# Kernel optimization log

Measured on AMD Instinct MI355X. Metric: run time of the kernel, lower is better.

## Reference

```python
import jax, jax.numpy as jnp
import numpy as np

B0, C0, H0, W0 = 2, 64, 48, 48
BR, DI, NS, RK, K = 128, 128, 16, 4, 4
EPS = 1e-5


def _bn_relu(x, g, b):
    # eval-mode BatchNorm2d (running mean 0, var 1) followed by ReLU; x is NCHW
    return jax.nn.relu(x * (g / jnp.sqrt(1.0 + EPS))[None, :, None, None] + b[None, :, None, None])


def _c1(x, w):
    # 1x1 conv, w: (O, C, 1, 1)
    return jnp.einsum('bchw,oc->bohw', x, w[:, :, 0, 0])


def _avgpool(x, k, s, p):
    # torch AvgPool2d with count_include_pad=True -> divide by k*k
    y = jax.lax.reduce_window(x, 0.0, jax.lax.add, (1, 1, k, k), (1, 1, s, s), ((0, 0), (0, 0), (p, p), (p, p)))
    return y / float(k * k)


def _resize(x, h, w):
    # bilinear, align_corners=False (half-pixel), NCHW
    return jax.image.resize(x, (x.shape[0], x.shape[1], h, w), 'bilinear')


def _pappm(x, s0_g, s0_b, s0_w, s1_g, s1_b, s1_w, s2_g, s2_b, s2_w, s3_g, s3_b, s3_w, s4_g, s4_b, s4_w, comp_g, comp_b, comp_w, sc_g, sc_b, sc_w):
    h, w = x.shape[2], x.shape[3]
    x0 = _c1(_bn_relu(x, s0_g, s0_b), s0_w)
    y1 = _c1(_bn_relu(_avgpool(x, 3, 1, 1), s1_g, s1_b), s1_w) + x0  # stride-1 pool keeps size
    y2 = _resize(_c1(_bn_relu(_avgpool(x, 5, 2, 2), s2_g, s2_b), s2_w), h, w) + x0
    y3 = _resize(_c1(_bn_relu(_avgpool(x, 9, 4, 4), s3_g, s3_b), s3_w), h, w) + x0
    y4 = _c1(_bn_relu(x.mean((2, 3), keepdims=True), s4_g, s4_b), s4_w) + x0  # 1x1 -> broadcast
    cat = jnp.concatenate([x0, y1, y2, y3, y4], axis=1)  # (B, 5*BR, H, W)
    comp = jax.lax.conv_general_dilated(_bn_relu(cat, comp_g, comp_b), comp_w, (1, 1), ((1, 1), (1, 1)), dimension_numbers=('NCHW', 'OIHW', 'NCHW'))
    return comp + _c1(_bn_relu(x, sc_g, sc_b), sc_w)


def _ss2d(xin, in_proj_w, dw_w, dw_b, x_proj_w, dt_w, dt_b, A_logs, Ds, ln_g, ln_b, out_proj_w):
    # xin: (B, H, W, d_model)
    Bb, Hh, Ww, _ = xin.shape
    xz = xin @ in_proj_w.T                      # (B,H,W,2*DI)
    xc, z = jnp.split(xz, 2, axis=-1)
    xc = jnp.transpose(xc, (0, 3, 1, 2))        # (B,DI,H,W)
    xc = jax.lax.conv_general_dilated(xc, dw_w, (1, 1), ((1, 1), (1, 1)), dimension_numbers=('NCHW', 'OIHW', 'NCHW'), feature_group_count=DI)
    xc = jax.nn.silu(xc + dw_b[None, :, None, None])
    L = Hh * Ww
    x_hw = xc.reshape(Bb, DI, L)
    x_wh = jnp.transpose(xc, (0, 1, 3, 2)).reshape(Bb, DI, L)
    xs = jnp.stack([x_hw, x_wh, x_hw[:, :, ::-1], x_wh[:, :, ::-1]], axis=1)  # (B,K,DI,L)
    x_dbl = jnp.einsum('bkdl,kcd->bkcl', xs, x_proj_w)
    dts, Bm, Cm = jnp.split(x_dbl, [RK, RK + NS], axis=2)  # (B,K,RK,L),(B,K,NS,L),(B,K,NS,L)
    delta = jax.nn.softplus(jnp.einsum('bkrl,kdr->bkdl', dts, dt_w) + dt_b[None, :, :, None])  # (B,K,DI,L)
    A = -jnp.exp(A_logs).reshape(K, DI, NS)
    a = jnp.exp(delta[..., None] * A[None, :, :, None, :])                    # (B,K,DI,L,NS)
    bu = (delta * xs)[..., None] * jnp.transpose(Bm, (0, 1, 3, 2))[:, :, None]  # (B,K,DI,L,NS)

    def comb(e1, e2):
        a1, b1 = e1
        a2, b2 = e2
        return a2 * a1, a2 * b1 + b2

    _, hst = jax.lax.associative_scan(comb, (a, bu), axis=3)  # h_t = a_t*h_{t-1} + b_t
    y = jnp.einsum('bkdln,bknl->bkdl', hst, Cm) + xs * Ds.reshape(K, DI)[None, :, :, None]
    inv = y[:, 2:4][:, :, :, ::-1]
    y3 = jnp.transpose(y[:, 1].reshape(Bb, DI, Ww, Hh), (0, 1, 3, 2)).reshape(Bb, DI, L)
    y4 = jnp.transpose(inv[:, 1].reshape(Bb, DI, Ww, Hh), (0, 1, 3, 2)).reshape(Bb, DI, L)
    ys = jnp.transpose(y[:, 0] + inv[:, 0] + y3 + y4, (0, 2, 1)).reshape(Bb, Hh, Ww, DI)
    mu = ys.mean(-1, keepdims=True)
    var = jnp.mean((ys - mu) ** 2, -1, keepdims=True)
    yn = (ys - mu) / jnp.sqrt(var + EPS) * ln_g + ln_b
    return (yn * jax.nn.silu(z)) @ out_proj_w.T  # (B,H,W,d_model)


def setup_inputs():
    key = jax.random.key(0)
    ks = iter(jax.random.split(key, 32))
    nrm = lambda shp, s: jax.random.normal(next(ks), shp, jnp.float32) * s
    d = {}
    d['x'] = nrm((B0, C0, H0, W0), 1.0)
    for nm in ['s0', 's1', 's2', 's3', 's4']:
        d[nm + '_g'] = jnp.ones((C0,), jnp.float32)
        d[nm + '_b'] = jnp.zeros((C0,), jnp.float32)
        d[nm + '_w'] = nrm((BR, C0, 1, 1), (2.0 / C0) ** 0.5)
    d['comp_g'] = jnp.ones((5 * BR,), jnp.float32)
    d['comp_b'] = jnp.zeros((5 * BR,), jnp.float32)
    d['comp_w'] = nrm((C0, 5 * BR, 3, 3), (2.0 / (5 * BR * 9)) ** 0.5)
    d['sc_g'] = jnp.ones((C0,), jnp.float32)
    d['sc_b'] = jnp.zeros((C0,), jnp.float32)
    d['sc_w'] = nrm((C0, C0, 1, 1), (2.0 / C0) ** 0.5)
    d['in_proj_w'] = nrm((2 * DI, C0), C0 ** -0.5)
    d['dw_w'] = nrm((DI, 1, 3, 3), 0.3)
    d['dw_b'] = jnp.zeros((DI,), jnp.float32)
    d['x_proj_w'] = nrm((K, RK + 2 * NS, DI), DI ** -0.5)
    d['dt_w'] = nrm((K, DI, RK), RK ** -0.5)
    d['dt_b'] = jnp.log(jnp.expm1(jnp.asarray(0.01, jnp.float32))) * jnp.ones((K, DI), jnp.float32)
    d['A_logs'] = jnp.tile(jnp.log(jnp.arange(1, NS + 1, dtype=jnp.float32))[None], (K * DI, 1))
    d['Ds'] = jnp.ones((K * DI,), jnp.float32)
    d['ln_g'] = jnp.ones((DI,), jnp.float32)
    d['ln_b'] = jnp.zeros((DI,), jnp.float32)
    d['out_proj_w'] = nrm((C0, DI), DI ** -0.5)
    d['fc1_w'] = nrm((BR, C0, 1, 1), C0 ** -0.5)
    d['fc1_b'] = jnp.zeros((BR,), jnp.float32)
    d['fc2_w'] = nrm((C0, BR, 1, 1), BR ** -0.5)
    d['fc2_b'] = jnp.zeros((C0,), jnp.float32)
    return d


def reference(x, s0_g, s0_b, s0_w, s1_g, s1_b, s1_w, s2_g, s2_b, s2_w, s3_g, s3_b, s3_w, s4_g, s4_b, s4_w, comp_g, comp_b, comp_w, sc_g, sc_b, sc_w, in_proj_w, dw_w, dw_b, x_proj_w, dt_w, dt_b, A_logs, Ds, ln_g, ln_b, out_proj_w, fc1_w, fc1_b, fc2_w, fc2_b):
    p = _pappm(x, s0_g, s0_b, s0_w, s1_g, s1_b, s1_w, s2_g, s2_b, s2_w, s3_g, s3_b, s3_w, s4_g, s4_b, s4_w, comp_g, comp_b, comp_w, sc_g, sc_b, sc_w)
    a = _ss2d(jnp.transpose(p, (0, 2, 3, 1)), in_proj_w, dw_w, dw_b, x_proj_w, dt_w, dt_b, A_logs, Ds, ln_g, ln_b, out_proj_w)
    x1 = jnp.transpose(a, (0, 3, 1, 2))  # (B,C0,H,W)
    h1 = jax.nn.silu(_c1(x1, fc1_w) + fc1_b[None, :, None, None])
    return _c1(h1, fc2_w) + fc2_b[None, :, None, None] + x1
```

## Files before the change

kernel.cpp:

```cpp
#include <hip/hip_runtime.h>
#include <math.h>

constexpr int cB = 2, cC = 64, cH = 48, cW = 48, cL = 48 * 48;
constexpr int cBR = 128, cDI = 128, cNS = 16, cRK = 4, cK = 4;
constexpr float cEPS = 1e-5f;
constexpr int NCH = 32;
constexpr int CHL = cL / NCH;
constexpr int KTOT = 5824;

typedef unsigned short u16;
typedef unsigned int u32;
typedef short s16x8 __attribute__((ext_vector_type(8)));
typedef float f32x4 __attribute__((ext_vector_type(4)));

__device__ __forceinline__ float bnrelu(float v, float g, float b) {
    float y = v * (g * rsqrtf(1.0f + cEPS)) + b;
    return y > 0.f ? y : 0.f;
}
__device__ __forceinline__ float silu(float v) {
    return v / (1.f + expf(-v));
}
__device__ __forceinline__ u16 f2bf(float f) {
    u32 u = __float_as_uint(f);
    u = (u + 0x7fffu + ((u >> 16) & 1u)) >> 16;
    return (u16)u;
}
__device__ __forceinline__ s16x8 cvt8(const float* p) {
    s16x8 r;
#pragma unroll
    for (int i = 0; i < 8; i++) r[i] = (short)f2bf(p[i]);
    return r;
}
__device__ __forceinline__ float row_sum16(float v) {
    v += __int_as_float(__builtin_amdgcn_update_dpp(0, __float_as_int(v), 0xB1, 0xF, 0xF, true));
    v += __int_as_float(__builtin_amdgcn_update_dpp(0, __float_as_int(v), 0x4E, 0xF, 0xF, true));
    v += __int_as_float(__builtin_amdgcn_update_dpp(0, __float_as_int(v), 0x124, 0xF, 0xF, true));
    v += __int_as_float(__builtin_amdgcn_update_dpp(0, __float_as_int(v), 0x128, 0xF, 0xF, true));
    return v;
}

__global__ void __launch_bounds__(256) k_pools(const float* __restrict__ x, float* __restrict__ pool3,
                                               float* __restrict__ pool5, float* __restrict__ pool9,
                                               float* __restrict__ gmean) {
    __shared__ float sm[4];
    int blk = blockIdx.x;
    int t = threadIdx.x;
    if (blk < 1152) {
        int idx = blk * 256 + t;
        int w = idx % cW, h = (idx / cW) % cH, bc = idx / cL;
        const float* p = x + bc * cL;
        float s = 0.f;
        for (int dh = -1; dh <= 1; dh++) {
            int hh = h + dh; if (hh < 0 || hh >= cH) continue;
            for (int dw = -1; dw <= 1; dw++) {
                int ww = w + dw; if (ww < 0 || ww >= cW) continue;
                s += p[hh * cW + ww];
            }
        }
        pool3[idx] = s * (1.f / 9.f);
    } else if (blk < 1440) {
        int idx = (blk - 1152) * 256 + t;
        int w = idx % 24, h = (idx / 24) % 24, bc = idx / 576;
        const float* p = x + bc * cL;
        float s = 0.f;
        for (int kh = 0; kh < 5; kh++) {
            int hh = h * 2 - 2 + kh; if (hh < 0 || hh >= cH) continue;
            for (int kw = 0; kw < 5; kw++) {
                int ww = w * 2 - 2 + kw; if (ww < 0 || ww >= cW) continue;
                s += p[hh * cW + ww];
            }
        }
        pool5[idx] = s * (1.f / 25.f);
    } else if (blk < 1512) {
        int idx = (blk - 1440) * 256 + t;
        int w = idx % 12, h = (idx / 12) % 12, bc = idx / 144;
        const float* p = x + bc * cL;
        float s = 0.f;
        for (int kh = 0; kh < 9; kh++) {
            int hh = h * 4 - 4 + kh; if (hh < 0 || hh >= cH) continue;
            for (int kw = 0; kw < 9; kw++) {
                int ww = w * 4 - 4 + kw; if (ww < 0 || ww >= cW) continue;
                s += p[hh * cW + ww];
            }
        }
        pool9[idx] = s * (1.f / 81.f);
    } else {
        int bc = blk - 1512;
        const float* p = x + bc * cL;
        float s = 0.f;
        for (int i = t; i < cL; i += 256) s += p[i];
        for (int m = 32; m > 0; m >>= 1) s += __shfl_down(s, m);
        if ((t & 63) == 0) sm[t >> 6] = s;
        __syncthreads();
        if (t == 0) gmean[bc] = (sm[0] + sm[1] + sm[2] + sm[3]) * (1.f / cL);
    }
}

__global__ void __launch_bounds__(256) k_prep(const float* __restrict__ cw, const float* __restrict__ scw,
                                              const float* __restrict__ s0w, const float* __restrict__ s1w,
                                              const float* __restrict__ ipw, const float* __restrict__ xpw,
                                              u16* __restrict__ w8, u16* __restrict__ wcat,
                                              u16* __restrict__ ipk, u16* __restrict__ xpk) {
    int blk = blockIdx.x, t = threadIdx.x;
    if (blk < 1456) {
        int idx = blk * 256 + t;
        int o = idx / KTOT, kx = idx % KTOT;
        float v;
        if (kx < 5760) { int tap = kx / 640, ch = kx % 640; v = cw[(o * 640 + ch) * 9 + tap]; }
        else v = scw[o * 64 + (kx - 5760)];
        w8[(((size_t)(kx >> 3) * 64) + o) * 8 + (kx & 7)] = f2bf(v);
    } else if (blk < 1520) {
        int idx = (blk - 1456) * 256 + t;
        int g = idx >> 13, r = idx & 8191;
        int o = r >> 6, c = r & 63;
        float v = (g ? s1w : s0w)[r];
        int kt = c >> 5, q = (c >> 3) & 3, j = c & 7, nt = o >> 4, ln = o & 15;
        wcat[(size_t)((((g * 2 + kt) * 4 + q) * 8 + nt) * 16 + ln) * 8 + j] = f2bf(v);
    } else if (blk < 1584) {
        int idx = (blk - 1520) * 256 + t;
        int o = idx >> 6, c = idx & 63;
        int kt = c >> 5, q = (c >> 3) & 3, j = c & 7, nt = o >> 4, ln = o & 15;
        ipk[(size_t)(((kt * 4 + q) * 16 + nt) * 16 + ln) * 8 + j] = f2bf(ipw[idx]);
    } else {
        int idx = (blk - 1584) * 256 + t;
        int o = idx >> 7, d = idx & 127;
        int kt = d >> 5, q = (d >> 3) & 3, j = d & 7, nt = o >> 4, ln = o & 15;
        xpk[(size_t)(((kt * 4 + q) * 9 + nt) * 16 + ln) * 8 + j] = f2bf(xpw[idx]);
    }
}

__global__ void __launch_bounds__(128) k_c1all(const float* __restrict__ pool5, const float* __restrict__ pool9,
                                               const float* __restrict__ gm,
                                               const float* __restrict__ s2g, const float* __restrict__ s2b,
                                               const float* __restrict__ s2w,
                                               const float* __restrict__ s3g, const float* __restrict__ s3b,
                                               const float* __restrict__ s3w,
                                               const float* __restrict__ s4g, const float* __restrict__ s4b,
                                               const float* __restrict__ s4w,
                                               float* __restrict__ c2cl, float* __restrict__ c3cl,
                                               float* __restrict__ c4) {
    int pos = blockIdx.x;
    const float *in, *g, *bb, *w;
    float* outp;
    int HW, b, pp;
    if (pos < cB * 576) { b = pos / 576; pp = pos % 576; in = pool5; g = s2g; bb = s2b; w = s2w; HW = 576; outp = c2cl + ((size_t)b * 576 + pp) * 128; }
    else if (pos < cB * 576 + cB * 144) { int r = pos - cB * 576; b = r / 144; pp = r % 144; in = pool9; g = s3g; bb = s3b; w = s3w; HW = 144; outp = c3cl + ((size_t)b * 144 + pp) * 128; }
    else { b = pos - cB * 576 - cB * 144; pp = 0; in = gm; g = s4g; bb = s4b; w = s4w; HW = 1; outp = c4 + (size_t)b * 128; }
    __shared__ float v[64];
    int t = threadIdx.x;
    if (t < 64) v[t] = bnrelu(in[(b * 64 + t) * HW + pp], g[t], bb[t]);
    __syncthreads();
    float acc = 0.f;
    const float* wr = w + t * 64;
#pragma unroll 16
    for (int c = 0; c < 64; c++) acc += v[c] * wr[c];
    outp[t] = acc;
}

__global__ void __launch_bounds__(256) k_cat2(
    const float* __restrict__ x, const float* __restrict__ pool3, const float* __restrict__ c4,
    const float* __restrict__ s0g, const float* __restrict__ s0b,
    const float* __restrict__ s1g, const float* __restrict__ s1b,
    const float* __restrict__ scg, const float* __restrict__ scb,
    const float* __restrict__ cg, const float* __restrict__ cbb,
    const u16* __restrict__ wcat, const float* __restrict__ c2cl, const float* __restrict__ c3cl,
    u16* __restrict__ catbf, u16* __restrict__ xbf) {
    int blk = blockIdx.x;
    int b = blk / 144;
    int l0 = (blk % 144) * 16;
    int t = threadIdx.x;
    __shared__ float axv[16][68];
    __shared__ float ap3[16][68];
    __shared__ u16 axc[16][66];
    int pc = t >> 4, p = t & 15;
#pragma unroll
    for (int i = 0; i < 4; i++) {
        int c = i * 16 + pc;
        float xraw = x[(size_t)(b * 64 + c) * cL + l0 + p];
        float p3raw = pool3[(size_t)(b * 64 + c) * cL + l0 + p];
        axv[p][c] = bnrelu(xraw, s0g[c], s0b[c]);
        ap3[p][c] = bnrelu(p3raw, s1g[c], s1b[c]);
        axc[p][c] = f2bf(bnrelu(xraw, scg[c], scb[c]));
    }
    __syncthreads();
#pragma unroll
    for (int i = 0; i < 4; i++) {
        int idx = i * 256 + t;
        int pp = idx >> 6, cc = idx & 63;
        xbf[((size_t)b * cL + l0 + pp) * 64 + cc] = axc[pp][cc];
    }
    int wv = t >> 6, lane = t & 63, ln = lane & 15, q = lane >> 4;
    f32x4 ax[2] = {};
    f32x4 ay[2] = {};
#pragma unroll
    for (int kt = 0; kt < 2; kt++) {
        s16x8 a0 = cvt8(&axv[ln][kt * 32 + q * 8]);
        s16x8 a1 = cvt8(&ap3[ln][kt * 32 + q * 8]);
#pragma unroll
        for (int jj = 0; jj < 2; jj++) {
            int nt = wv * 2 + jj;
            s16x8 b0 = *(const s16x8*)(wcat + (size_t)((((0 * 2 + kt) * 4 + q) * 8 + nt) * 16 + ln) * 8);
            s16x8 b1 = *(const s16x8*)(wcat + (size_t)((((1 * 2 + kt) * 4 + q) * 8 + nt) * 16 + ln) * 8);
            ax[jj] = __builtin_amdgcn_mfma_f32_16x16x32_bf16(a0, b0, ax[jj], 0, 0, 0);
            ay[jj] = __builtin_amdgcn_mfma_f32_16x16x32_bf16(a1, b1, ay[jj], 0, 0, 0);
        }
    }
    int hrow = l0 / cW, w0g = l0 % cW;
    float sy2 = hrow * 0.5f - 0.25f;
    float fy2 = floorf(sy2); int iy2 = (int)fy2; float ay2 = sy2 - fy2;
    int y20 = min(max(iy2, 0), 23), y21 = min(max(iy2 + 1, 0), 23);
    float sy3 = hrow * 0.25f - 0.375f;
    float fy3 = floorf(sy3); int iy3 = (int)fy3; float ay3 = sy3 - fy3;
    int y30 = min(max(iy3, 0), 11), y31 = min(max(iy3 + 1, 0), 11);
    const float* c2b = c2cl + (size_t)b * 576 * 128;
    const float* c3b = c3cl + (size_t)b * 144 * 128;
#pragma unroll
    for (int r = 0; r < 4; r++) {
        int pp = q * 4 + r;
        int wq = w0g + pp;
        float sx2 = wq * 0.5f - 0.25f;
        float fx2 = floorf(sx2); int ix2 = (int)fx2; float ax2 = sx2 - fx2;
        int x20 = min(max(ix2, 0), 23), x21 = min(max(ix2 + 1, 0), 23);
        float sx3 = wq * 0.25f - 0.375f;
        float fx3 = floorf(sx3); int ix3 = (int)fx3; float ax3 = sx3 - fx3;
        int x30 = min(max(ix3, 0), 11), x31 = min(max(ix3 + 1, 0), 11);
#pragma unroll
        for (int jj = 0; jj < 2; jj++) {
            int ch = (wv * 2 + jj) * 16 + ln;
            float v00 = c2b[(y20 * 24 + x20) * 128 + ch], v01 = c2b[(y20 * 24 + x21) * 128 + ch];
            float v10 = c2b[(y21 * 24 + x20) * 128 + ch], v11 = c2b[(y21 * 24 + x21) * 128 + ch];
            float t0 = v00 + (v01 - v00) * ax2, t1 = v10 + (v11 - v10) * ax2;
            float u2v = t0 + (t1 - t0) * ay2;
            float w00 = c3b[(y30 * 12 + x30) * 128 + ch], w01 = c3b[(y30 * 12 + x31) * 128 + ch];
            float w10 = c3b[(y31 * 12 + x30) * 128 + ch], w11 = c3b[(y31 * 12 + x31) * 128 + ch];
            float s0_ = w00 + (w01 - w00) * ax3, s1_ = w10 + (w11 - w10) * ax3;
            float u3v = s0_ + (s1_ - s0_) * ay3;
            float x0 = ax[jj][r];
            float y1 = ay[jj][r] + x0;
            float y2 = x0 + u2v;
            float y3 = x0 + u3v;
            float y4 = x0 + c4[b * 128 + ch];
            u16* base = catbf + ((size_t)b * cL + l0 + pp) * 640;
            base[ch]       = f2bf(bnrelu(x0, cg[ch],       cbb[ch]));
            base[128 + ch] = f2bf(bnrelu(y1, cg[128 + ch], cbb[128 + ch]));
            base[256 + ch] = f2bf(bnrelu(y2, cg[256 + ch], cbb[256 + ch]));
            base[384 + ch] = f2bf(bnrelu(y3, cg[384 + ch], cbb[384 + ch]));
            base[512 + ch] = f2bf(bnrelu(y4, cg[512 + ch], cbb[512 + ch]));
        }
    }
}

__global__ void __launch_bounds__(64) k_comp(const u16* __restrict__ catbf,
                                             const u16* __restrict__ xbf,
                                             const u16* __restrict__ w8,
                                             float* __restrict__ part) {
    int blk = blockIdx.x;
    int slice = blk % 9;
    int pxt = blk / 9;
    int pix0 = pxt * 16;
    int b = pix0 / cL;
    int lane = threadIdx.x;
    int ln = lane & 15, q = lane >> 4;
    int la = (pix0 + ln) - b * cL;
    int h = la / cW, w = la % cW;
    int kh = slice / 3 - 1, kw = slice % 3 - 1;
    int hh = h + kh, ww = w + kw;
    bool ok = (hh >= 0) && (hh < cH) && (ww >= 0) && (ww < cW);
    const u16* ap = catbf + ((size_t)b * cL + hh * cW + ww) * 640 + q * 8;
    f32x4 acc[4] = {};
    int kb = slice * 640;
#pragma unroll 4
    for (int cc = 0; cc < 20; cc++) {
        s16x8 av;
        if (ok) av = *(const s16x8*)(ap + cc * 32);
        else av = s16x8{0, 0, 0, 0, 0, 0, 0, 0};
        const u16* wrow = w8 + (((size_t)((kb + cc * 32) >> 3) + q) * 64) * 8;
#pragma unroll
        for (int j = 0; j < 4; j++) {
            s16x8 bv = *(const s16x8*)(wrow + (size_t)(j * 16 + ln) * 8);
            acc[j] = __builtin_amdgcn_mfma_f32_16x16x32_bf16(av, bv, acc[j], 0, 0, 0);
        }
    }
    if (slice == 4) {
        const u16* xp = xbf + (size_t)(pix0 + ln) * 64 + q * 8;
#pragma unroll
        for (int cc = 0; cc < 2; cc++) {
            s16x8 av = *(const s16x8*)(xp + cc * 32);
            const u16* wrow = w8 + (((size_t)((5760 + cc * 32) >> 3) + q) * 64) * 8;
#pragma unroll
            for (int j = 0; j < 4; j++) {
                s16x8 bv = *(const s16x8*)(wrow + (size_t)(j * 16 + ln) * 8);
                acc[j] = __builtin_amdgcn_mfma_f32_16x16x32_bf16(av, bv, acc[j], 0, 0, 0);
            }
        }
    }
    float* pb = part + ((size_t)slice * (cB * cL) + pix0) * 64;
#pragma unroll
    for (int j = 0; j < 4; j++) {
#pragma unroll
        for (int r = 0; r < 4; r++) {
            pb[(size_t)(q * 4 + r) * 64 + j * 16 + ln] = acc[j][r];
        }
    }
}

__global__ void __launch_bounds__(256) k_ip(const float* __restrict__ part, const u16* __restrict__ ipk,
                                            float* __restrict__ xc, float* __restrict__ z) {
    int px0 = blockIdx.x * 16;
    int t = threadIdx.x;
    __shared__ float pv[16][68];
#pragma unroll
    for (int i = 0; i < 4; i++) {
        int idx = i * 256 + t;
        int p = idx >> 6, c = idx & 63;
        float s = 0.f;
#pragma unroll
        for (int sl = 0; sl < 9; sl++)
            s += part[((size_t)sl * (cB * cL) + px0 + p) * 64 + c];
        pv[p][c] = s;
    }
    __syncthreads();
    int wv = t >> 6, lane = t & 63, ln = lane & 15, q = lane >> 4;
    f32x4 acc[4] = {};
#pragma unroll
    for (int kt = 0; kt < 2; kt++) {
        s16x8 a = cvt8(&pv[ln][kt * 32 + q * 8]);
#pragma unroll
        for (int jn = 0; jn < 4; jn++) {
            int nt = wv * 4 + jn;
            s16x8 bfr = *(const s16x8*)(ipk + (size_t)(((kt * 4 + q) * 16 + nt) * 16 + ln) * 8);
            acc[jn] = __builtin_amdgcn_mfma_f32_16x16x32_bf16(a, bfr, acc[jn], 0, 0, 0);
        }
    }
#pragma unroll
    for (int jn = 0; jn < 4; jn++) {
        int o = (wv * 4 + jn) * 16 + ln;
#pragma unroll
        for (int r = 0; r < 4; r++) {
            int p = q * 4 + r;
            if (o < 128) xc[((size_t)px0 + p) * 128 + o] = acc[jn][r];
            else         z[((size_t)px0 + p) * 128 + (o - 128)] = acc[jn][r];
        }
    }
}

__global__ void k_dw(const float* __restrict__ xc, const float* __restrict__ dww,
                     const float* __restrict__ dwb, float* __restrict__ xca) {
    int idx = blockIdx.x * 256 + threadIdx.x;
    if (idx >= cB * cL * cDI) return;
    int d = idx & 127;
    int rest = idx >> 7;
    int l = rest % cL, b = rest / cL;
    int h = l / cW, w = l % cW;
    const float* base = xc + (size_t)b * cL * 128 + d;
    float acc = dwb[d];
    const float* kw = dww + d * 9;
    for (int i = 0; i < 3; i++) {
        int hh = h + i - 1; if (hh < 0 || hh >= cH) continue;
        for (int j = 0; j < 3; j++) {
            int ww = w + j - 1; if (ww < 0 || ww >= cW) continue;
            acc += base[(size_t)(hh * cW + ww) * 128] * kw[i * 3 + j];
        }
    }
    xca[idx] = silu(acc);
}

__global__ void __launch_bounds__(1024) k_xdbl4(const float* __restrict__ xca, const u16* __restrict__ xpk,
                                                const float* __restrict__ dtw, const float* __restrict__ dtb,
                                                float* __restrict__ bc, float* __restrict__ delta) {
    int blk = blockIdx.x;
    int b = blk / 144;
    int l0 = (blk % 144) * 16;
    int t = threadIdx.x;
    __shared__ float av[16][132];
    __shared__ float Dt[16][148];
#pragma unroll
    for (int i = 0; i < 2; i++) {
        int id = i * 1024 + t;
        int d = id & 127, p = id >> 7;
        av[p][d] = xca[((size_t)b * cL + l0 + p) * 128 + d];
    }
    __syncthreads();
    int wv = t >> 6, lane = t & 63, ln = lane & 15, q = lane >> 4;
    if (wv < 9) {
        int nt = wv;
        f32x4 acc = {};
#pragma unroll
        for (int kt = 0; kt < 4; kt++) {
            s16x8 a = cvt8(&av[ln][kt * 32 + q * 8]);
            s16x8 bfr = *(const s16x8*)(xpk + (size_t)(((kt * 4 + q) * 9 + nt) * 16 + ln) * 8);
            acc = __builtin_amdgcn_mfma_f32_16x16x32_bf16(a, bfr, acc, 0, 0, 0);
        }
#pragma unroll
        for (int r = 0; r < 4; r++)
            Dt[q * 4 + r][nt * 16 + ln] = acc[r];
    }
    __syncthreads();
#pragma unroll
    for (int i = 0; i < 2; i++) {
        int id = i * 1024 + t;
        int cc = id & 31, kk = (id >> 5) & 3, p = id >> 7;
        bc[((size_t)(b * 4 + kk) * cL + l0 + p) * 32 + cc] = Dt[p][kk * 36 + 4 + cc];
    }
    {
        int d = t & 127;
        int kk = (t >> 7) & 3;
        int p0 = t >> 9;
        const float* wd = dtw + (size_t)(kk * 128 + d) * 4;
        float w0 = wd[0], w1 = wd[1], w2 = wd[2], w3 = wd[3];
        float bb = dtb[kk * 128 + d];
        float* dout = delta + ((size_t)(b * 4 + kk) * cL + l0) * 128 + d;
#pragma unroll
        for (int i = 0; i < 8; i++) {
            int p = p0 + i * 2;
            float pre = bb + w0 * Dt[p][kk * 36] + w1 * Dt[p][kk * 36 + 1]
                      + w2 * Dt[p][kk * 36 + 2] + w3 * Dt[p][kk * 36 + 3];
            float dl = pre > 20.f ? pre : log1pf(expf(pre));
            dout[(size_t)p * 128] = dl;
        }
    }
}

__device__ __forceinline__ int xs_index(int k, int l) {
    int lp = (k & 2) ? (cL - 1 - l) : l;
    if (k & 1) { int w = lp / cH, h = lp % cH; return h * cW + w; }
    return lp;
}

__global__ void __launch_bounds__(256) k_scan1(const float* __restrict__ delta, const float* __restrict__ xca,
                                               const float* __restrict__ bc, const float* __restrict__ Alogs,
                                               float* __restrict__ Pend, float* __restrict__ hend) {
    int blk = blockIdx.x;
    int c = blk & 31;
    if (c == NCH - 1) return;
    int g = blk >> 5;
    int dgq = g & 7, bk = g >> 3;
    int k = bk & 3, b = bk >> 2;
    int t = threadIdx.x;
    int n = t & 15;
    int d = dgq * 16 + (t >> 4);
    float A = -expf(Alogs[(k * 128 + d) * 16 + n]);
    const float* dp = delta + (size_t)bk * cL * 128 + d;
    const float* xp = xca + (size_t)b * cL * 128 + d;
    const float* bp = bc + (size_t)bk * cL * 32 + n;
    int off = xs_index(k, c * CHL);
    int step = (k == 0) ? 1 : (k == 1) ? cW : (k == 2) ? -1 : -cW;
    float P = 1.f, h = 0.f;
#pragma unroll 4
    for (int i = 0; i < CHL; i++) {
        float dl = dp[(size_t)off * 128];
        float a = expf(dl * A);
        h = a * h + dl * xp[(size_t)off * 128] * bp[(size_t)off * 32];
        P *= a;
        off += step;
        if (off >= cL) off -= (cL - 1);
        else if (off < 0) off += (cL - 1);
    }
    Pend[(size_t)blk * 256 + t] = P;
    hend[(size_t)blk * 256 + t] = h;
}

__global__ void __launch_bounds__(256) k_scan2(const float* __restrict__ Pend, float* __restrict__ hend) {
    int id = blockIdx.x * 256 + threadIdx.x;
    int t = id & 255;
    int g = id >> 8;
    float h = 0.f;
    for (int c = 0; c < NCH; c++) {
        size_t idx = ((size_t)g * NCH + c) * 256 + t;
        float tmp = hend[idx];
        float Pv = Pend[idx];
        hend[idx] = h;
        h = Pv * h + tmp;
    }
}

__global__ void __launch_bounds__(256) k_scan3(const float* __restrict__ delta, const float* __restrict__ xca,
                                               const float* __restrict__ bc, const float* __restrict__ Alogs,
                                               const float* __restrict__ Dsv, const float* __restrict__ hinb,
                                               float* __restrict__ y) {
    int blk = blockIdx.x;
    int c = blk & 31;
    int g = blk >> 5;
    int dgq = g & 7, bk = g >> 3;
    int k = bk & 3, b = bk >> 2;
    int t = threadIdx.x;
    int n = t & 15;
    int d = dgq * 16 + (t >> 4);
    float A = -expf(Alogs[(k * 128 + d) * 16 + n]);
    float Dsd = Dsv[k * 128 + d];
    const float* dp = delta + (size_t)bk * cL * 128 + d;
    const float* xp = xca + (size_t)b * cL * 128 + d;
    const float* bp = bc + (size_t)bk * cL * 32 + n;
    const float* cp = bc + (size_t)bk * cL * 32 + 16 + n;
    float* yb = y + (size_t)bk * cL * 128 + d;
    int off = xs_index(k, c * CHL);
    int step = (k == 0) ? 1 : (k == 1) ? cW : (k == 2) ? -1 : -cW;
    float h = hinb[(size_t)blk * 256 + t];
#pragma unroll 2
    for (int i = 0; i < CHL; i++) {
        float dl = dp[(size_t)off * 128];
        float xv = xp[(size_t)off * 128];
        float a = expf(dl * A);
        h = a * h + dl * xv * bp[(size_t)off * 32];
        float contrib = row_sum16(h * cp[(size_t)off * 32]);
        if (n == 0) yb[(size_t)off * 128] = contrib + xv * Dsd;
        off += step;
        if (off >= cL) off -= (cL - 1);
        else if (off < 0) off += (cL - 1);
    }
}

__global__ void __launch_bounds__(256) k_tail(const float* __restrict__ y, const float* __restrict__ z,
                                              const float* __restrict__ lng, const float* __restrict__ lnb,
                                              const float* __restrict__ opw,
                                              const float* __restrict__ f1w, const float* __restrict__ f1b,
                                              const float* __restrict__ f2w, const float* __restrict__ f2b,
                                              float* __restrict__ out) {
    int blk = blockIdx.x;
    int b = blk / 144;
    int l0 = (blk % 144) * 16;
    int t = threadIdx.x;
    __shared__ float v[16][132];
    __shared__ float x1s[16][68];
    __shared__ float h1s[16][132];
    __shared__ float mus[16], rss[16];
    const float* yb = y + (size_t)b * 4 * cL * 128;
#pragma unroll
    for (int i = 0; i < 8; i++) {
        int id = i * 256 + t;
        int d = id & 127, p = id >> 7;
        size_t base = (size_t)(l0 + p) * 128 + d;
        v[p][d] = yb[base] + yb[(size_t)cL * 128 + base] + yb[(size_t)2 * cL * 128 + base] + yb[(size_t)3 * cL * 128 + base];
    }
    __syncthreads();
    {
        int p = t >> 4, c8 = (t & 15) * 8;
        float s = 0.f;
#pragma unroll
        for (int j = 0; j < 8; j++) s += v[p][c8 + j];
        s = row_sum16(s);
        float mu = s * (1.f / 128.f);
        float s2 = 0.f;
#pragma unroll
        for (int j = 0; j < 8; j++) { float dv = v[p][c8 + j] - mu; s2 += dv * dv; }
        s2 = row_sum16(s2);
        if ((t & 15) == 0) { mus[p] = mu; rss[p] = rsqrtf(s2 * (1.f / 128.f) + cEPS); }
    }
    __syncthreads();
#pragma unroll
    for (int i = 0; i < 8; i++) {
        int id = i * 256 + t;
        int d = id & 127, p = id >> 7;
        float zz = z[((size_t)b * cL + l0 + p) * 128 + d];
        v[p][d] = ((v[p][d] - mus[p]) * rss[p] * lng[d] + lnb[d]) * silu(zz);
    }
    __syncthreads();
#pragma unroll
    for (int i = 0; i < 4; i++) {
        int id = i * 256 + t;
        int p = id & 15, o = id >> 4;
        const float* wr = opw + o * 128;
        float acc = 0.f;
#pragma unroll 16
        for (int d2 = 0; d2 < 128; d2++) acc += v[p][d2] * wr[d2];
        x1s[p][o] = acc;
    }
    __syncthreads();
#pragma unroll
    for (int i = 0; i < 8; i++) {
        int id = i * 256 + t;
        int p = id & 15, j = id >> 4;
        const float* wr = f1w + j * 64;
        float acc = f1b[j];
#pragma unroll 16
        for (int c = 0; c < 64; c++) acc += x1s[p][c] * wr[c];
        h1s[p][j] = silu(acc);
    }
    __syncthreads();
#pragma unroll
    for (int i = 0; i < 4; i++) {
        int id = i * 256 + t;
        int p = id & 15, o = id >> 4;
        const float* wr = f2w + o * 128;
        float acc = f2b[o];
#pragma unroll 16
        for (int j = 0; j < 128; j++) acc += h1s[p][j] * wr[j];
        out[((size_t)b * 64 + o) * cL + l0 + p] = acc + x1s[p][o];
    }
}

extern "C" void kernel_launch(void* const* d_in, const int* in_sizes, int n_in,
                              void* d_out, int out_size, void* d_ws, size_t ws_size,
                              hipStream_t stream) {
    (void)in_sizes; (void)n_in; (void)out_size; (void)ws_size;
    const float* x    = (const float*)d_in[0];
    const float* s0g  = (const float*)d_in[1];
    const float* s0b  = (const float*)d_in[2];
    const float* s0w  = (const float*)d_in[3];
    const float* s1g  = (const float*)d_in[4];
    const float* s1b  = (const float*)d_in[5];
    const float* s1w  = (const float*)d_in[6];
    const float* s2g  = (const float*)d_in[7];
    const float* s2b  = (const float*)d_in[8];
    const float* s2w  = (const float*)d_in[9];
    const float* s3g  = (const float*)d_in[10];
    const float* s3b  = (const float*)d_in[11];
    const float* s3w  = (const float*)d_in[12];
    const float* s4g  = (const float*)d_in[13];
    const float* s4b  = (const float*)d_in[14];
    const float* s4w  = (const float*)d_in[15];
    const float* cg   = (const float*)d_in[16];
    const float* cbb  = (const float*)d_in[17];
    const float* cw   = (const float*)d_in[18];
    const float* scg  = (const float*)d_in[19];
    const float* scb  = (const float*)d_in[20];
    const float* scw  = (const float*)d_in[21];
    const float* ipw  = (const float*)d_in[22];
    const float* dww  = (const float*)d_in[23];
    const float* dwb  = (const float*)d_in[24];
    const float* xpw  = (const float*)d_in[25];
    const float* dtw  = (const float*)d_in[26];
    const float* dtb  = (const float*)d_in[27];
    const float* Alog = (const float*)d_in[28];
    const float* Dsv  = (const float*)d_in[29];
    const float* lng  = (const float*)d_in[30];
    const float* lnb  = (const float*)d_in[31];
    const float* opw  = (const float*)d_in[32];
    const float* f1w  = (const float*)d_in[33];
    const float* f1b  = (const float*)d_in[34];
    const float* f2w  = (const float*)d_in[35];
    const float* f2b  = (const float*)d_in[36];
    float* out = (float*)d_out;

    float* ws = (float*)d_ws;
    size_t off = 0;
    float* pool3  = ws + off; off += 294912;
    float* pool5  = ws + off; off += 73728;
    float* pool9  = ws + off; off += 18432;
    float* gmean  = ws + off; off += 128;
    float* c2cl   = ws + off; off += 147456;
    float* c3cl   = ws + off; off += 36864;
    float* c4     = ws + off; off += 256;
    u16*   catbf  = (u16*)(ws + off); off += 1474560;
    u16*   xbf    = (u16*)(ws + off); off += 147456;
    u16*   w8     = (u16*)(ws + off); off += 186368;
    u16*   wcat   = (u16*)(ws + off); off += 8192;
    u16*   ipk    = (u16*)(ws + off); off += 8192;
    float* xc     = ws + off; off += 589824;
    u16*   xpk    = (u16*)(ws + off); off += 9216;
    float* xca    = ws + off; off += 589824;
    float* zbuf   = ws + off; off += 589824;
    float* bcbuf  = ws + off; off += 589824;
    float* Pend   = ws + off; off += 524288;
    float* ybuf   = ws + off; off += 2359296;
    off += 294912;
    float* delta  = ws + 0;
    float* hend   = xc;
    float* part   = ybuf;

    k_pools<<<1640, 256, 0, stream>>>(x, pool3, pool5, pool9, gmean);
    k_prep<<<1656, 256, 0, stream>>>(cw, scw, s0w, s1w, ipw, xpw, w8, wcat, ipk, xpk);
    k_c1all<<<cB * 576 + cB * 144 + cB, 128, 0, stream>>>(pool5, pool9, gmean, s2g, s2b, s2w,
                                                          s3g, s3b, s3w, s4g, s4b, s4w, c2cl, c3cl, c4);
    k_cat2<<<cB * 144, 256, 0, stream>>>(x, pool3, c4, s0g, s0b, s1g, s1b, scg, scb, cg, cbb,
                                         wcat, c2cl, c3cl, catbf, xbf);
    k_comp<<<(cB * cL / 16) * 9, 64, 0, stream>>>(catbf, xbf, w8, part);
    k_ip<<<cB * cL / 16, 256, 0, stream>>>(part, ipk, xc, zbuf);
    k_dw<<<(cB * cL * 128 + 255) / 256, 256, 0, stream>>>(xc, dww, dwb, xca);
    k_xdbl4<<<cB * 144, 1024, 0, stream>>>(xca, xpk, dtw, dtb, bcbuf, delta);
    k_scan1<<<64 * NCH, 256, 0, stream>>>(delta, xca, bcbuf, Alog, Pend, hend);
    k_scan2<<<64, 256, 0, stream>>>(Pend, hend);
    k_scan3<<<64 * NCH, 256, 0, stream>>>(delta, xca, bcbuf, Alog, Dsv, hend, ybuf);
    k_tail<<<cB * 144, 256, 0, stream>>>(ybuf, zbuf, lng, lnb, opw, f1w, f1b, f2w, f2b, out);
}
```

Before: 302.9 us.

## Fuse 3x3 comp conv with in_proj via in-block split-K reduction; halve tail tile

Merges the 3x3 compression conv and the in_proj GEMM into one kernel. Each 512-thread block splits the 182 K-steps across 8 waves, reduces the partial results in shared memory, and feeds the bf16 sum straight into the in_proj MFMAs. This removes the global partial-sum buffer round trip and one launch. Separately, the tail kernel now handles 8 pixels per block instead of 16, doubling the block count for better occupancy, with half the threads idle in the LayerNorm step.

```diff
diff --git a/kernel.cpp b/kernel.cpp
--- a/kernel.cpp
+++ b/kernel.cpp
@@ -250,96 +250,81 @@
     }
 }
 
-__global__ void __launch_bounds__(64) k_comp(const u16* __restrict__ catbf,
-                                             const u16* __restrict__ xbf,
-                                             const u16* __restrict__ w8,
-                                             float* __restrict__ part) {
-    int blk = blockIdx.x;
-    int slice = blk % 9;
-    int pxt = blk / 9;
-    int pix0 = pxt * 16;
+__global__ void __launch_bounds__(512) k_compip(const u16* __restrict__ catbf,
+                                                const u16* __restrict__ xbf,
+                                                const u16* __restrict__ w8,
+                                                const u16* __restrict__ ipk,
+                                                float* __restrict__ xc, float* __restrict__ z) {
+    int pix0 = blockIdx.x * 16;
     int b = pix0 / cL;
-    int lane = threadIdx.x;
-    int ln = lane & 15, q = lane >> 4;
+    int t = threadIdx.x;
+    int wv = t >> 6, lane = t & 63, ln = lane & 15, q = lane >> 4;
+    __shared__ float pl[8][16][68];
+    __shared__ u16 pv16[16][72];
     int la = (pix0 + ln) - b * cL;
     int h = la / cW, w = la % cW;
-    int kh = slice / 3 - 1, kw = slice % 3 - 1;
-    int hh = h + kh, ww = w + kw;
-    bool ok = (hh >= 0) && (hh < cH) && (ww >= 0) && (ww < cW);
-    const u16* ap = catbf + ((size_t)b * cL + hh * cW + ww) * 640 + q * 8;
     f32x4 acc[4] = {};
-    int kb = slice * 640;
-#pragma unroll 4
-    for (int cc = 0; cc < 20; cc++) {
+    int ks0 = wv * 23;
+    int kcnt = (wv == 7) ? 21 : 23;
+    for (int i = 0; i < kcnt; i++) {
+        int ks = ks0 + i;
         s16x8 av;
-        if (ok) av = *(const s16x8*)(ap + cc * 32);
-        else av = s16x8{0, 0, 0, 0, 0, 0, 0, 0};
-        const u16* wrow = w8 + (((size_t)((kb + cc * 32) >> 3) + q) * 64) * 8;
+        if (ks < 180) {
+            int s = ks / 20;
+            int cc = ks - s * 20;
+            int s3 = s / 3;
+            int kh = s3 - 1, kw = s - s3 * 3 - 1;
+            int hh = h + kh, ww = w + kw;
+            bool ok = (hh >= 0) && (hh < cH) && (ww >= 0) && (ww < cW);
+            const u16* ap = catbf + (((size_t)b * cL + hh * cW + ww) * 640 + cc * 32 + q * 8);
+            if (ok) av = *(const s16x8*)ap;
+            else av = s16x8{0, 0, 0, 0, 0, 0, 0, 0};
+        } else {
+            int cc = ks - 180;
+            av = *(const s16x8*)(xbf + (size_t)(pix0 + ln) * 64 + cc * 32 + q * 8);
+        }
+        const u16* wrow = w8 + ((size_t)ks * 4 + q) * 512;
 #pragma unroll
         for (int j = 0; j < 4; j++) {
             s16x8 bv = *(const s16x8*)(wrow + (size_t)(j * 16 + ln) * 8);
             acc[j] = __builtin_amdgcn_mfma_f32_16x16x32_bf16(av, bv, acc[j], 0, 0, 0);
         }
     }
-    if (slice == 4) {
-        const u16* xp = xbf + (size_t)(pix0 + ln) * 64 + q * 8;
-#pragma unroll
-        for (int cc = 0; cc < 2; cc++) {
-            s16x8 av = *(const s16x8*)(xp + cc * 32);
-            const u16* wrow = w8 + (((size_t)((5760 + cc * 32) >> 3) + q) * 64) * 8;
-#pragma unroll
-            for (int j = 0; j < 4; j++) {
-                s16x8 bv = *(const s16x8*)(wrow + (size_t)(j * 16 + ln) * 8);
-                acc[j] = __builtin_amdgcn_mfma_f32_16x16x32_bf16(av, bv, acc[j], 0, 0, 0);
-            }
-        }
-    }
-    float* pb = part + ((size_t)slice * (cB * cL) + pix0) * 64;
-#pragma unroll
-    for (int j = 0; j < 4; j++) {
-#pragma unroll
-        for (int r = 0; r < 4; r++) {
-            pb[(size_t)(q * 4 + r) * 64 + j * 16 + ln] = acc[j][r];
-        }
-    }
-}
-
-__global__ void __launch_bounds__(256) k_ip(const float* __restrict__ part, const u16* __restrict__ ipk,
-                                            float* __restrict__ xc, float* __restrict__ z) {
-    int px0 = blockIdx.x * 16;
-    int t = threadIdx.x;
-    __shared__ float pv[16][68];
-#pragma unroll
-    for (int i = 0; i < 4; i++) {
-        int idx = i * 256 + t;
-        int p = idx >> 6, c = idx & 63;
+#pragma unroll
+    for (int j = 0; j < 4; j++)
+#pragma unroll
+        for (int r = 0; r < 4; r++)
+            pl[wv][q * 4 + r][j * 16 + ln] = acc[j][r];
+    __syncthreads();
+#pragma unroll
+    for (int e = 0; e < 2; e++) {
+        int id = e * 512 + t;
+        int p = id >> 6, c = id & 63;
         float s = 0.f;
 #pragma unroll
-        for (int sl = 0; sl < 9; sl++)
-            s += part[((size_t)sl * (cB * cL) + px0 + p) * 64 + c];
-        pv[p][c] = s;
-    }
-    __syncthreads();
-    int wv = t >> 6, lane = t & 63, ln = lane & 15, q = lane >> 4;
-    f32x4 acc[4] = {};
+        for (int w2 = 0; w2 < 8; w2++) s += pl[w2][p][c];
+        pv16[p][c] = f2bf(s);
+    }
+    __syncthreads();
+    f32x4 a2[2] = {};
 #pragma unroll
     for (int kt = 0; kt < 2; kt++) {
-        s16x8 a = cvt8(&pv[ln][kt * 32 + q * 8]);
-#pragma unroll
-        for (int jn = 0; jn < 4; jn++) {
-            int nt = wv * 4 + jn;
+        s16x8 a = *(const s16x8*)(&pv16[ln][kt * 32 + q * 8]);
+#pragma unroll
+        for (int jn = 0; jn < 2; jn++) {
+            int nt = wv * 2 + jn;
             s16x8 bfr = *(const s16x8*)(ipk + (size_t)(((kt * 4 + q) * 16 + nt) * 16 + ln) * 8);
-            acc[jn] = __builtin_amdgcn_mfma_f32_16x16x32_bf16(a, bfr, acc[jn], 0, 0, 0);
-        }
-    }
-#pragma unroll
-    for (int jn = 0; jn < 4; jn++) {
-        int o = (wv * 4 + jn) * 16 + ln;
+            a2[jn] = __builtin_amdgcn_mfma_f32_16x16x32_bf16(a, bfr, a2[jn], 0, 0, 0);
+        }
+    }
+#pragma unroll
+    for (int jn = 0; jn < 2; jn++) {
+        int o = (wv * 2 + jn) * 16 + ln;
 #pragma unroll
         for (int r = 0; r < 4; r++) {
             int p = q * 4 + r;
-            if (o < 128) xc[((size_t)px0 + p) * 128 + o] = acc[jn][r];
-            else         z[((size_t)px0 + p) * 128 + (o - 128)] = acc[jn][r];
+            if (o < 128) xc[((size_t)pix0 + p) * 128 + o] = a2[jn][r];
+            else         z[((size_t)pix0 + p) * 128 + (o - 128)] = a2[jn][r];
         }
     }
 }
@@ -517,23 +502,23 @@
                                               const float* __restrict__ f2w, const float* __restrict__ f2b,
                                               float* __restrict__ out) {
     int blk = blockIdx.x;
-    int b = blk / 144;
-    int l0 = (blk % 144) * 16;
-    int t = threadIdx.x;
-    __shared__ float v[16][132];
-    __shared__ float x1s[16][68];
-    __shared__ float h1s[16][132];
-    __shared__ float mus[16], rss[16];
+    int b = blk / 288;
+    int l0 = (blk % 288) * 8;
+    int t = threadIdx.x;
+    __shared__ float v[8][132];
+    __shared__ float x1s[8][68];
+    __shared__ float h1s[8][132];
+    __shared__ float mus[8], rss[8];
     const float* yb = y + (size_t)b * 4 * cL * 128;
 #pragma unroll
-    for (int i = 0; i < 8; i++) {
+    for (int i = 0; i < 4; i++) {
         int id = i * 256 + t;
         int d = id & 127, p = id >> 7;
         size_t base = (size_t)(l0 + p) * 128 + d;
         v[p][d] = yb[base] + yb[(size_t)cL * 128 + base] + yb[(size_t)2 * cL * 128 + base] + yb[(size_t)3 * cL * 128 + base];
     }
     __syncthreads();
-    {
+    if (t < 128) {
         int p = t >> 4, c8 = (t & 15) * 8;
         float s = 0.f;
 #pragma unroll
@@ -548,7 +533,7 @@
     }
     __syncthreads();
 #pragma unroll
-    for (int i = 0; i < 8; i++) {
+    for (int i = 0; i < 4; i++) {
         int id = i * 256 + t;
         int d = id & 127, p = id >> 7;
         float zz = z[((size_t)b * cL + l0 + p) * 128 + d];
@@ -556,9 +541,9 @@
     }
     __syncthreads();
 #pragma unroll
-    for (int i = 0; i < 4; i++) {
+    for (int i = 0; i < 2; i++) {
         int id = i * 256 + t;
-        int p = id & 15, o = id >> 4;
+        int p = id & 7, o = id >> 3;
         const float* wr = opw + o * 128;
         float acc = 0.f;
 #pragma unroll 16
@@ -567,9 +552,9 @@
     }
     __syncthreads();
 #pragma unroll
-    for (int i = 0; i < 8; i++) {
+    for (int i = 0; i < 4; i++) {
         int id = i * 256 + t;
-        int p = id & 15, j = id >> 4;
+        int p = id & 7, j = id >> 3;
         const float* wr = f1w + j * 64;
         float acc = f1b[j];
 #pragma unroll 16
@@ -578,9 +563,9 @@
     }
     __syncthreads();
 #pragma unroll
-    for (int i = 0; i < 4; i++) {
+    for (int i = 0; i < 2; i++) {
         int id = i * 256 + t;
-        int p = id & 15, o = id >> 4;
+        int p = id & 7, o = id >> 3;
         const float* wr = f2w + o * 128;
         float acc = f2b[o];
 #pragma unroll 16
@@ -656,7 +641,6 @@
     off += 294912;
     float* delta  = ws + 0;
     float* hend   = xc;
-    float* part   = ybuf;
 
     k_pools<<<1640, 256, 0, stream>>>(x, pool3, pool5, pool9, gmean);
     k_prep<<<1656, 256, 0, stream>>>(cw, scw, s0w, s1w, ipw, xpw, w8, wcat, ipk, xpk);
@@ -664,12 +648,11 @@
                                                           s3g, s3b, s3w, s4g, s4b, s4w, c2cl, c3cl, c4);
     k_cat2<<<cB * 144, 256, 0, stream>>>(x, pool3, c4, s0g, s0b, s1g, s1b, scg, scb, cg, cbb,
                                          wcat, c2cl, c3cl, catbf, xbf);
-    k_comp<<<(cB * cL / 16) * 9, 64, 0, stream>>>(catbf, xbf, w8, part);
-    k_ip<<<cB * cL / 16, 256, 0, stream>>>(part, ipk, xc, zbuf);
+    k_compip<<<cB * cL / 16, 512, 0, stream>>>(catbf, xbf, w8, ipk, xc, zbuf);
     k_dw<<<(cB * cL * 128 + 255) / 256, 256, 0, stream>>>(xc, dww, dwb, xca);
     k_xdbl4<<<cB * 144, 1024, 0, stream>>>(xca, xpk, dtw, dtb, bcbuf, delta);
     k_scan1<<<64 * NCH, 256, 0, stream>>>(delta, xca, bcbuf, Alog, Pend, hend);
     k_scan2<<<64, 256, 0, stream>>>(Pend, hend);
     k_scan3<<<64 * NCH, 256, 0, stream>>>(delta, xca, bcbuf, Alog, Dsv, hend, ybuf);
-    k_tail<<<cB * 144, 256, 0, stream>>>(ybuf, zbuf, lng, lnb, opw, f1w, f1b, f2w, f2b, out);
-}
+    k_tail<<<cB * 288, 256, 0, stream>>>(ybuf, zbuf, lng, lnb, opw, f1w, f1b, f2w, f2b, out);
+}
```

Result: no change. 302.8 us (-0.0%).
